# Optimization experiments

Hardware: AMD Instinct MI355X
Metric: run time of the kernel (lower is better)

## Reference

```python
import jax, jax.numpy as jnp
import numpy as np

N = 50000   # nodes
E = 400000  # edges (before self-loops)
F = 128     # num_features
H = 8       # heads (layer 1)
C = 64      # hidden_channels
B = 64      # graphs in batch
K = 10      # num_classes
NEG_SLOPE = 0.2


def setup_inputs() -> dict:
    key = jax.random.key(0)
    ks = jax.random.split(key, 12)
    g = lambda k, shape, fan: jax.random.normal(k, shape, jnp.float32) / np.sqrt(fan).astype(np.float32)
    return {
        "x": jax.random.normal(ks[0], (N, F), jnp.float32),
        "edge_index": jax.random.randint(ks[1], (2, E), 0, N, jnp.int32),
        "batch": jnp.sort(jax.random.randint(ks[2], (N,), 0, B, jnp.int32)),
        "W1": g(ks[3], (F, H * C), F),
        "att_src1": g(ks[4], (H, C), C),
        "att_dst1": g(ks[5], (H, C), C),
        "b1": jnp.zeros((H * C,), jnp.float32),
        "W2": g(ks[6], (H * C, C), H * C),
        "att_src2": g(ks[7], (1, C), C),
        "att_dst2": g(ks[8], (1, C), C),
        "b2": jnp.zeros((C,), jnp.float32),
        "lin1_w": g(ks[9], (C, C), C),
        "lin1_b": jnp.zeros((C,), jnp.float32),
        "lin2_w": g(ks[10], (C, K), C),
        "lin2_b": jnp.zeros((K,), jnp.float32),
    }


def gat_conv(x, src, dst, W, att_src, att_dst, bias):
    """PyG GATConv (self-loops already appended to src/dst). x:[N,Fin] -> [N,H*C]."""
    heads, out_c = att_src.shape
    h = (x @ W).reshape(N, heads, out_c)                      # [N,H,C]
    a_s = jnp.einsum('nhc,hc->nh', h, att_src)                # [N,H]
    a_d = jnp.einsum('nhc,hc->nh', h, att_dst)
    e = jax.nn.leaky_relu(a_s[src] + a_d[dst], NEG_SLOPE)     # [E',H]
    # segment softmax over incoming edges of each destination node
    m = jax.ops.segment_max(e, dst, num_segments=N)
    e = jnp.exp(e - m[dst])
    denom = jax.ops.segment_sum(e, dst, num_segments=N)
    alpha = e / (denom[dst] + 1e-16)                          # [E',H]
    out = jax.ops.segment_sum(h[src] * alpha[:, :, None], dst, num_segments=N)  # [N,H,C]
    return out.reshape(N, heads * out_c) + bias


def reference(x, edge_index, batch, W1, att_src1, att_dst1, b1,
              W2, att_src2, att_dst2, b2, lin1_w, lin1_b, lin2_w, lin2_b):
    loops = jnp.arange(N, dtype=edge_index.dtype)
    src = jnp.concatenate([edge_index[0], loops])
    dst = jnp.concatenate([edge_index[1], loops])

    h = gat_conv(x, src, dst, W1, att_src1, att_dst1, b1)     # [N, H*C]
    h = jax.nn.elu(h)                                         # dropout inactive (eval)
    h = gat_conv(h, src, dst, W2, att_src2, att_dst2, b2)     # [N, C]
    h = jax.nn.elu(h)

    pooled = jax.ops.segment_sum(h, batch, num_segments=B)    # global_add_pool -> [B, C]
    z = jax.nn.elu(pooled @ lin1_w + lin1_b)
    logits = z @ lin2_w + lin2_b
    return jax.nn.log_softmax(logits, axis=-1)
```

## Files before the change

### kernel.cpp

```cpp
#include <hip/hip_runtime.h>
#include <hip/hip_bf16.h>

#define DEV static __device__ __forceinline__

constexpr int F1 = 128;
constexpr int H1 = 8;
constexpr int C  = 64;
constexpr int B  = 64;
constexpr int K  = 10;
constexpr float NEG = 0.2f;
constexpr unsigned SMASK = 0x07FFFFFFu;

typedef __attribute__((ext_vector_type(8))) short short8;
typedef __attribute__((ext_vector_type(4))) float floatx4;

DEV float b2f(__hip_bfloat16 x) { return __bfloat162float(x); }
DEV float elu1(float v) { return v > 0.f ? v : (__expf(v) - 1.f); }
DEV unsigned short f2bbits(float f) {
  __hip_bfloat16 b = __float2bfloat16(f);
  return *(unsigned short*)&b;
}
DEV float blo(unsigned u) { return __uint_as_float(u << 16); }
DEV float bhi(unsigned u) { return __uint_as_float(u & 0xffff0000u); }
DEV float bu(unsigned short u) { return __uint_as_float(((unsigned)u) << 16); }
DEV unsigned pack2(float lo, float hi) {
  return (unsigned)f2bbits(lo) | ((unsigned)f2bbits(hi) << 16);
}
DEV float rcp_nr(float x) {
  float r = __builtin_amdgcn_rcpf(x);
  return r * (2.f - x * r);
}


DEV int detect_dev(const void* xraw, int* lds) {
  if (threadIdx.x == 0) {
    const __hip_bfloat16* xb = (const __hip_bfloat16*)xraw;
    int bad = 0;
    for (int i = 0; i < 128; ++i) {
      float v = b2f(xb[2 * i]);
      if (!(fabsf(v) < 1e4f)) bad++;
    }
    *lds = (bad < 13) ? 1 : 0;
  }
  __syncthreads();
  return *lds;
}

#define CVT(p, i) (isbf ? b2f(((const __hip_bfloat16*)(p))[i]) : ((const float*)(p))[i])

__global__ void fused_prep_kernel(const void* x_raw, const void* w1raw,
                                  const void* as1r, const void* ad1r, const void* b1r,
                                  const void* w2raw,
                                  const void* as2r, const void* ad2r, const void* b2r,
                                  const void* l1wr, const void* l1br,
                                  const void* l2wr, const void* l2br,
                                  unsigned short* __restrict__ xbf,
                                  unsigned short* __restrict__ w1frag,
                                  unsigned short* __restrict__ w2frag,
                                  unsigned short* __restrict__ vfrag,
                                  float* __restrict__ wts,
                                  int* __restrict__ deg,
                                  float* __restrict__ pooled,
                                  int nX, int N) {
  __shared__ int fl;
  int isbf = detect_dev(x_raw, &fl);
  int gid = blockIdx.x * 256 + threadIdx.x;
  int stride = gridDim.x * 256;

  int ng = nX >> 3;
  if (isbf) {
    const uint4* src = (const uint4*)x_raw;
    uint4* dst = (uint4*)xbf;
    for (int i = gid; i < ng; i += stride) dst[i] = src[i];
  } else {
    const float4* src = (const float4*)x_raw;
    uint4* dst = (uint4*)xbf;
    for (int i = gid; i < ng; i += stride) {
      float4 a = src[2 * i], b = src[2 * i + 1];
      uint4 o;
      o.x = pack2(a.x, a.y); o.y = pack2(a.z, a.w);
      o.z = pack2(b.x, b.y); o.w = pack2(b.z, b.w);
      dst[i] = o;
    }
  }
  for (int i = ng * 8 + gid; i < nX; i += stride)
    xbf[i] = isbf ? ((const unsigned short*)x_raw)[i]
                  : f2bbits(((const float*)x_raw)[i]);

  for (int i = gid; i < 512;  i += stride) {
    int hp = i >> 7, l16 = (i >> 3) & 15, nt = i & 7;
    int c = hp * 128 + nt * 16 + l16;
    wts[1024 + i] = CVT(b1r, c);
  }
  for (int i = gid; i < 64;   i += stride) wts[1536 + i] = CVT(as2r, i);
  for (int i = gid; i < 64;   i += stride) wts[1600 + i] = CVT(ad2r, i);
  for (int i = gid; i < 64;   i += stride) wts[1664 + i] = CVT(b2r, i);
  for (int i = gid; i < 4096; i += stride) wts[1728 + i] = CVT(l1wr, i);
  for (int i = gid; i < 64;   i += stride) wts[5824 + i] = CVT(l1br, i);
  for (int i = gid; i < 640;  i += stride) wts[5888 + i] = CVT(l2wr, i);
  for (int i = gid; i < 10;   i += stride) wts[6528 + i] = CVT(l2br, i);
  for (int t = gid; t < 8192; t += stride) {
    int lane = t & 63, ks = (t >> 6) & 3, nt = t >> 8;
    for (int j = 0; j < 8; ++j) {
      int k = ks * 32 + (lane >> 4) * 8 + j;
      int n = nt * 16 + (lane & 15);
      w1frag[t * 8 + j] = f2bbits(CVT(w1raw, k * 512 + n));
    }
  }
  for (int t = gid; t < 4096; t += stride) {
    int lane = t & 63, nt = (t >> 6) & 3, ks = t >> 8;
    for (int j = 0; j < 8; ++j) {
      int p = ks * 32 + (lane >> 4) * 8 + j;
      int hp = p >> 7, pl16 = (p >> 3) & 15, pnt = p & 7;
      int k = hp * 128 + pnt * 16 + pl16;
      int n = nt * 16 + (lane & 15);
      w2frag[t * 8 + j] = f2bbits(CVT(w2raw, k * 64 + n));
    }
  }
  for (int t = gid; t < 2048; t += stride) {
    int j = t & 7, lane = (t >> 3) & 63, ks = t >> 9;
    int k = ks * 32 + (lane >> 4) * 8 + j;
    int n = lane & 15;
    int hh = (n < 8) ? n : (n - 8);
    float s = 0.f;
    if (n < 8) {
      for (int c = 0; c < 64; ++c)
        s += CVT(w1raw, k * 512 + hh * 64 + c) * CVT(as1r, hh * 64 + c);
    } else {
      for (int c = 0; c < 64; ++c)
        s += CVT(w1raw, k * 512 + hh * 64 + c) * CVT(ad1r, hh * 64 + c);
    }
    vfrag[(ks * 64 + lane) * 8 + j] = f2bbits(s);
  }
  for (int i = gid; i < N; i += stride) deg[i] = 0;
  for (int i = gid; i < B * C; i += stride) pooled[i] = 0.f;
}

__global__ __launch_bounds__(256) void deg_att_kernel(
    const int* __restrict__ ei, int E, int Etot, int* __restrict__ deg,
    const unsigned short* __restrict__ xbf,
    const unsigned short* __restrict__ vfrag,
    float* __restrict__ a_s, float* __restrict__ a_d,
    int N, int attBlocks) {
  if ((int)blockIdx.x >= attBlocks) {
    int e = ((int)blockIdx.x - attBlocks) * 256 + threadIdx.x;
    if (e < Etot) {
      int d = (e < E) ? ei[E + e] : e - E;
      atomicAdd(&deg[d], 1);
    }
    return;
  }
  int t = threadIdx.x, w = t >> 6, lane = t & 63;
  int quad = lane >> 4, l16 = lane & 15;
  int row0 = blockIdx.x * 64 + w * 16;

  floatx4 acc = {};
  int rl = row0 + l16; if (rl >= N) rl = N - 1;
  const unsigned short* xp = xbf + (size_t)rl * 128 + quad * 8;
#pragma unroll
  for (int ks = 0; ks < 4; ++ks) {
    short8 a = *(const short8*)(xp + ks * 32);
    short8 b = *(const short8*)&vfrag[(ks * 64 + lane) * 8];
    acc = __builtin_amdgcn_mfma_f32_16x16x32_bf16(a, b, acc, 0, 0, 0);
  }
#pragma unroll
  for (int r = 0; r < 4; ++r) {
    int row = row0 + quad * 4 + r;
    if (row < N) {
      if (l16 < 8) a_s[(size_t)row * 8 + l16] = acc[r];
      else         a_d[(size_t)row * 8 + (l16 - 8)] = acc[r];
    }
  }
}

__global__ void scan_block_kernel(const int* __restrict__ deg,
                                  int* __restrict__ local,
                                  int* __restrict__ bsum, int N) {
  __shared__ int tmp[256];
  int t = threadIdx.x;
  int i = blockIdx.x * 256 + t;
  int v = (i < N) ? deg[i] : 0;
  tmp[t] = v;
  __syncthreads();
  for (int off = 1; off < 256; off <<= 1) {
    int u = (t >= off) ? tmp[t - off] : 0;
    __syncthreads();
    tmp[t] += u;
    __syncthreads();
  }
  if (i < N) local[i] = tmp[t] - v;
  if (t == 255) bsum[blockIdx.x] = tmp[255];
}

__global__ void scan_finish_kernel(const int* __restrict__ local,
                                   const int* __restrict__ bsum, int nb,
                                   int* __restrict__ rowptr,
                                   int* __restrict__ cursor, int N, int Etot) {
  __shared__ int tmp[256];
  __shared__ int offs;
  int t = threadIdx.x;
  int v0 = (t < nb) ? bsum[t] : 0;
  tmp[t] = v0;
  __syncthreads();
  for (int off = 1; off < 256; off <<= 1) {
    int u = (t >= off) ? tmp[t - off] : 0;
    __syncthreads();
    tmp[t] += u;
    __syncthreads();
  }
  if (t == (int)blockIdx.x) offs = tmp[t] - v0;
  __syncthreads();
  int i = blockIdx.x * 256 + t;
  if (i < N) {
    int r = local[i] + offs;
    rowptr[i] = r;
    cursor[i] = r;
  }
  if (i == 0) rowptr[N] = Etot;
}

__global__ void fill_weight_kernel(const int* __restrict__ ei, int E, int Etot,
                                   const float* __restrict__ a_s,
                                   const float* __restrict__ a_d,
                                   int* __restrict__ cursor,
                                   int* __restrict__ col,
                                   unsigned short* __restrict__ wedge) {
  int e = blockIdx.x * 256 + threadIdx.x;
  if (e >= Etot) return;
  int s, d;
  if (e < E) { s = ei[e]; d = ei[E + e]; } else { s = d = e - E; }
  int pos = atomicAdd(&cursor[d], 1);
  col[pos] = s | ((d & 15) << 27);
  float4 s0 = *(const float4*)(a_s + (size_t)s * 8);
  float4 s1 = *(const float4*)(a_s + (size_t)s * 8 + 4);
  float4 d0 = *(const float4*)(a_d + (size_t)d * 8);
  float4 d1 = *(const float4*)(a_d + (size_t)d * 8 + 4);
  float v, w0, w1, w2, w3, w4, w5, w6, w7;
  v = s0.x + d0.x; v = v > 0.f ? v : NEG * v; w0 = __expf(v);
  v = s0.y + d0.y; v = v > 0.f ? v : NEG * v; w1 = __expf(v);
  v = s0.z + d0.z; v = v > 0.f ? v : NEG * v; w2 = __expf(v);
  v = s0.w + d0.w; v = v > 0.f ? v : NEG * v; w3 = __expf(v);
  v = s1.x + d1.x; v = v > 0.f ? v : NEG * v; w4 = __expf(v);
  v = s1.y + d1.y; v = v > 0.f ? v : NEG * v; w5 = __expf(v);
  v = s1.z + d1.z; v = v > 0.f ? v : NEG * v; w6 = __expf(v);
  v = s1.w + d1.w; v = v > 0.f ? v : NEG * v; w7 = __expf(v);
  uint4 o;
  o.x = pack2(w0, w1); o.y = pack2(w2, w3);
  o.z = pack2(w4, w5); o.w = pack2(w6, w7);
  *(uint4*)(wedge + (size_t)pos * 8) = o;
}

__global__ __launch_bounds__(512, 6) void aggx_gemm12_kernel(
    const unsigned short* __restrict__ xbf,
    const unsigned short* __restrict__ W1frag,
    const int* __restrict__ rowptr,
    const int* __restrict__ col,
    const unsigned short* __restrict__ wedge,
    const float* __restrict__ bias_perm,
    const unsigned short* __restrict__ W2frag,
    const float* __restrict__ att_src2,
    const float* __restrict__ att_dst2,
    unsigned short* __restrict__ h2,
    float* __restrict__ a_s2, float* __restrict__ a_d2,
    int N) {
  __shared__ __align__(16) char LB[8 * 16 * 136 * 2];

  int t = threadIdx.x, w = t >> 6, lane = t & 63;
  int q = lane >> 4, n = lane & 15;
  int dbase = blockIdx.x * 16;

  int R0 = rowptr[dbase];
  int R1 = rowptr[min(dbase + 16, N)];
  int nch = (R1 - R0 + 31) >> 5;

  int kp = t >> 5, pp = t & 31;
  int skey = (pp & 7) << 4;
  int dw = t >> 5, kw = t & 31;

  short8 onesf = {};
  if (n == 0) {
#pragma unroll
    for (int j = 0; j < 8; ++j) onesf[j] = (short)0x3F80;
  }

  floatx4 accw[8] = {};
  floatx4 accdn = {};

  uint2 pxa, pxb;
  uint4 pwv;
  int pcv;
  {
    int e0 = R0 + 2 * kp;
    int ec0 = min(e0, R1 - 1), ec1 = min(e0 + 1, R1 - 1);
    int s0 = col[ec0] & SMASK;
    int s1 = col[ec1] & SMASK;
    pxa = *(const uint2*)(xbf + (size_t)s0 * 128 + pp * 4);
    pxb = *(const uint2*)(xbf + (size_t)s1 * 128 + pp * 4);
    int ew = min(R0 + kw, R1 - 1);
    pcv = col[ew];
    pwv = *(const uint4*)(wedge + (size_t)ew * 8);
  }

  for (int c = 0; c < nch; ++c) {
    char* Lb = LB + (c & 1) * 16384;
    unsigned short* XgTc = (unsigned short*)Lb;
    unsigned short* Wmc  = (unsigned short*)(Lb + 8192);

    {
      int base = 256 * pp + 4 * kp;
      unsigned w0 = (pxa.x & 0xffffu) | (pxb.x << 16);
      unsigned w1 = (pxa.x >> 16) | (pxb.x & 0xffff0000u);
      unsigned w2 = (pxa.y & 0xffffu) | (pxb.y << 16);
      unsigned w3 = (pxa.y >> 16) | (pxb.y & 0xffff0000u);
      *(unsigned*)(Lb + ((base)       ^ skey)) = w0;
      *(unsigned*)(Lb + ((base + 64)  ^ skey)) = w1;
      *(unsigned*)(Lb + ((base + 128) ^ skey)) = w2;
      *(unsigned*)(Lb + ((base + 192) ^ skey)) = w3;

      int ew = R0 + c * 32 + kw;
      int dl = (pcv >> 27) & 15;
      bool mine = (ew < R1) && (dl == dw);
      unsigned short* wmp = Wmc + dw * 32 + kw;
      wmp[0]    = mine ? (unsigned short)(pwv.x & 0xffff) : 0;
      wmp[512]  = mine ? (unsigned short)(pwv.x >> 16)    : 0;
      wmp[1024] = mine ? (unsigned short)(pwv.y & 0xffff) : 0;
      wmp[1536] = mine ? (unsigned short)(pwv.y >> 16)    : 0;
      wmp[2048] = mine ? (unsigned short)(pwv.z & 0xffff) : 0;
      wmp[2560] = mine ? (unsigned short)(pwv.z >> 16)    : 0;
      wmp[3072] = mine ? (unsigned short)(pwv.w & 0xffff) : 0;
      wmp[3584] = mine ? (unsigned short)(pwv.w >> 16)    : 0;
    }
    if (c + 1 < nch) {
      int ebase = R0 + (c + 1) * 32;
      int e0 = ebase + 2 * kp;
      int ec0 = min(e0, R1 - 1), ec1 = min(e0 + 1, R1 - 1);
      int s0 = col[ec0] & SMASK;
      int s1 = col[ec1] & SMASK;
      pxa = *(const uint2*)(xbf + (size_t)s0 * 128 + pp * 4);
      pxb = *(const uint2*)(xbf + (size_t)s1 * 128 + pp * 4);
      int ew = min(ebase + kw, R1 - 1);
      pcv = col[ew];
      pwv = *(const uint4*)(wedge + (size_t)ew * 8);
    }
    __syncthreads();

    short8 af = *(const short8*)(Wmc + w * 512 + n * 32 + 8 * q);
    accdn = __builtin_amdgcn_mfma_f32_16x16x32_bf16(af, onesf, accdn, 0, 0, 0);
#pragma unroll
    for (int ft = 0; ft < 8; ++ft) {
      int f = ft * 16 + n;
      int bb = f * 64 + 16 * q;
      bb ^= ((f >> 2) & 7) << 4;
      short8 bfr = *(const short8*)((const char*)XgTc + bb);
      accw[ft] = __builtin_amdgcn_mfma_f32_16x16x32_bf16(af, bfr, accw[ft], 0, 0, 0);
    }
  }

  __syncthreads();

  unsigned short* AggP = (unsigned short*)LB;
  {
    float dnv[4];
#pragma unroll
    for (int r = 0; r < 4; ++r) {
      float dr = __shfl(accdn[r], lane & 48);
      dnv[r] = rcp_nr(dr + 1e-16f);
    }
#pragma unroll
    for (int ft = 0; ft < 8; ++ft)
#pragma unroll
      for (int r = 0; r < 4; ++r)
        AggP[w * 2176 + (4 * q + r) * 136 + ft * 16 + n] =
            f2bbits(accw[ft][r] * dnv[r]);
  }
  __syncthreads();

  int hp = w >> 1, qq = w & 1;
  floatx4 acc2[4] = {};
  {
    const unsigned short* Bp = W1frag + (size_t)hp * 16384;
#pragma unroll
    for (int ks = 0; ks < 4; ++ks) {
      short8 a2 = *(const short8*)&AggP[w * 2176 + n * 136 + ks * 32 + q * 8];
#pragma unroll
      for (int j = 0; j < 4; ++j) {
        int nt = qq * 4 + j;
        short8 b2 = *(const short8*)&Bp[((nt * 4 + ks) * 64 + lane) * 8];
        acc2[j] = __builtin_amdgcn_mfma_f32_16x16x32_bf16(a2, b2, acc2[j], 0, 0, 0);
      }
    }
  }
  float4 bq = *(const float4*)&bias_perm[hp * 128 + n * 8 + qq * 4];
  __syncthreads();

  unsigned short* O1 = (unsigned short*)LB;
  float* RED = (float*)(LB + 16640);
  float* PSb = (float*)(LB + 20736);
  float* PDb = (float*)(LB + 20800);

  {
#pragma unroll
    for (int r = 0; r < 4; ++r) {
      int dl = 4 * q + r;
      uint2 ov;
      ov.x = pack2(elu1(acc2[0][r] + bq.x), elu1(acc2[1][r] + bq.y));
      ov.y = pack2(elu1(acc2[2][r] + bq.z), elu1(acc2[3][r] + bq.w));
      *(uint2*)(O1 + dl * 520 + hp * 128 + n * 8 + qq * 4) = ov;
    }
    if (t < 32) ((float*)(LB + 20736))[t] = 0.f;
  }
  __syncthreads();

  int nt2 = w & 3, kh = w >> 2;
  floatx4 acc3 = {};
#pragma unroll
  for (int ks8 = 0; ks8 < 8; ++ks8) {
    int ks = kh * 8 + ks8;
    short8 a3 = *(const short8*)&O1[n * 520 + ks * 32 + q * 8];
    short8 b3 = *(const short8*)&W2frag[((ks * 4 + nt2) * 64 + lane) * 8];
    acc3 = __builtin_amdgcn_mfma_f32_16x16x32_bf16(a3, b3, acc3, 0, 0, 0);
  }
  if (kh == 1) *(floatx4*)&RED[(nt2 * 64 + lane) * 4] = acc3;
  __syncthreads();

  if (kh == 0) {
    floatx4 other = *(const floatx4*)&RED[(nt2 * 64 + lane) * 4];
    float asw = att_src2[nt2 * 16 + n];
    float adw = att_dst2[nt2 * 16 + n];
    float ps[4], pd[4];
#pragma unroll
    for (int r = 0; r < 4; ++r) {
      float v = acc3[r] + other[r];
      int row = dbase + 4 * q + r;
      if (row < N) h2[(size_t)row * 64 + nt2 * 16 + n] = f2bbits(v);
      ps[r] = v * asw;
      pd[r] = v * adw;
    }
#pragma unroll
    for (int r = 0; r < 4; ++r) {
      float p = ps[r], qd = pd[r];
#pragma unroll
      for (int off2 = 1; off2 < 16; off2 <<= 1) {
        p += __shfl_xor(p, off2);
        qd += __shfl_xor(qd, off2);
      }
      if (n == 0) {
        int dl = 4 * q + r;
        atomicAdd(&PSb[dl], p);
        atomicAdd(&PDb[dl], qd);
      }
    }
  }
  __syncthreads();
  if (t < 16) {
    int row = dbase + t;
    if (row < N) {
      a_s2[row] = PSb[t];
      a_d2[row] = PDb[t];
    }
  }
}

__global__ __launch_bounds__(256) void gat_agg1_pool_kernel(
    const int* __restrict__ rowptr,
    const int* __restrict__ col,
    const float* __restrict__ a_s,
    const float* __restrict__ a_d,
    const unsigned short* __restrict__ hfeat,
    const float* __restrict__ bias,
    const int* __restrict__ batch,
    float* __restrict__ pooled, int N) {
  __shared__ float S[16][64];
  int wave = threadIdx.x >> 6, lane = threadIdx.x & 63;
  int qg = lane >> 4, l16 = lane & 15;
  int base = blockIdx.x * 16;
  const uint2* hfu = (const uint2*)hfeat;
  float4 bb = ((const float4*)bias)[l16];

  for (int j = 0; j < 4; ++j) {
    int d = base + wave * 4 + j;
    if (d < N) {
      int beg = rowptr[d], end = rowptr[d + 1];
      float adv = a_d[d];
      float acc0 = 0.f, acc1 = 0.f, acc2 = 0.f, acc3 = 0.f, wsum = 0.f;
#pragma unroll 2
      for (int i = beg + qg; i < end; i += 4) {
        int s = col[i] & SMASK;
        float v = a_s[s] + adv;
        v = v > 0.f ? v : NEG * v;
        float wv = __expf(v);
        wsum += wv;
        uint2 u = hfu[(size_t)s * 16 + l16];
        acc0 += wv * blo(u.x); acc1 += wv * bhi(u.x);
        acc2 += wv * blo(u.y); acc3 += wv * bhi(u.y);
      }
#pragma unroll
      for (int off = 16; off <= 32; off <<= 1) {
        acc0 += __shfl_xor(acc0, off); acc1 += __shfl_xor(acc1, off);
        acc2 += __shfl_xor(acc2, off); acc3 += __shfl_xor(acc3, off);
        wsum += __shfl_xor(wsum, off);
      }
      float winv = 1.f / (wsum + 1e-16f);
      if (qg == 0) {
        int dl = wave * 4 + j;
        S[dl][4 * l16 + 0] = bu(f2bbits(elu1(acc0 * winv + bb.x)));
        S[dl][4 * l16 + 1] = bu(f2bbits(elu1(acc1 * winv + bb.y)));
        S[dl][4 * l16 + 2] = bu(f2bbits(elu1(acc2 * winv + bb.z)));
        S[dl][4 * l16 + 3] = bu(f2bbits(elu1(acc3 * winv + bb.w)));
      }
    }
  }
  __syncthreads();

  if (threadIdx.x < 64) {
    int ch = threadIdx.x;
    int cnt = min(16, N - base);
    if (cnt > 0) {
      int cur = batch[base];
      float acc = 0.f;
      for (int nn = 0; nn < cnt; ++nn) {
        int bn = batch[base + nn];
        if (bn != cur) {
          unsafeAtomicAdd(&pooled[cur * 64 + ch], acc);
          acc = 0.f; cur = bn;
        }
        acc += S[nn][ch];
      }
      unsafeAtomicAdd(&pooled[cur * 64 + ch], acc);
    }
  }
}

__global__ void head_kernel(const float* __restrict__ pooled,
                            const float* __restrict__ lin1_w,
                            const float* __restrict__ lin1_b,
                            const float* __restrict__ lin2_w,
                            const float* __restrict__ lin2_b,
                            const void* __restrict__ x_raw,
                            void* __restrict__ outv) {
  __shared__ float P[C];
  __shared__ float Zs[C];
  __shared__ float Ls[K];
  __shared__ float lse_s;
  __shared__ int fl;
  int isbf = detect_dev(x_raw, &fl);
  int g = blockIdx.x, t = threadIdx.x;
  P[t] = pooled[g * C + t];
  __syncthreads();
  float acc = lin1_b[t];
  for (int k = 0; k < C; ++k) acc += P[k] * lin1_w[k * C + t];
  Zs[t] = elu1(acc);
  __syncthreads();
  if (t < K) {
    float a = lin2_b[t];
    for (int k = 0; k < C; ++k) a += Zs[k] * lin2_w[k * K + t];
    Ls[t] = a;
  }
  __syncthreads();
  if (t == 0) {
    float mx = -1e30f;
    for (int c = 0; c < K; ++c) mx = fmaxf(mx, Ls[c]);
    float s = 0.f;
    for (int c = 0; c < K; ++c) s += __expf(Ls[c] - mx);
    lse_s = mx + __logf(s);
  }
  __syncthreads();
  if (t < K) {
    float val = Ls[t] - lse_s;
    if (isbf) ((__hip_bfloat16*)outv)[g * K + t] = __float2bfloat16(val);
    else      ((float*)outv)[g * K + t] = val;
  }
}

extern "C" void kernel_launch(void* const* d_in, const int* in_sizes, int n_in,
                              void* d_out, int out_size, void* d_ws, size_t ws_size,
                              hipStream_t stream) {
  const void* x_raw = d_in[0];
  const int*  ei    = (const int*)d_in[1];
  const int*  batch = (const int*)d_in[2];

  const int N    = in_sizes[2];
  const int E    = in_sizes[1] / 2;
  const int Etot = E + N;
  const int nb   = (N + 255) / 256;

  float* ws   = (float*)d_ws;
  size_t off  = 0;

  float* wts = ws + off; off += 6544;
  float* b1w  = wts + 1024;
  float* as2w = wts + 1536;
  float* ad2w = wts + 1600;
  float* b2w  = wts + 1664;
  float* l1w  = wts + 1728;
  float* l1b  = wts + 5824;
  float* l2w  = wts + 5888;
  float* l2b  = wts + 6528;

  unsigned short* xbf    = (unsigned short*)(ws + off); off += (size_t)N * 64;
  unsigned short* w1frag = (unsigned short*)(ws + off); off += 32768;
  unsigned short* w2frag = (unsigned short*)(ws + off); off += 16384;
  unsigned short* vfrag  = (unsigned short*)(ws + off); off += 1024;
  unsigned short* wedge  = (unsigned short*)(ws + off); off += (size_t)Etot * 4;
  unsigned short* h2bf   = (unsigned short*)(ws + off); off += (size_t)N * 32;
  float* as1  = ws + off; off += (size_t)N * H1;
  float* ad1  = ws + off; off += (size_t)N * H1;
  float* as2  = ws + off; off += (size_t)N;
  float* ad2  = ws + off; off += (size_t)N;
  float* pooled = ws + off; off += (size_t)B * C;

  int* ibase  = (int*)(ws + off);
  int* deg    = ibase;                 ibase += N;
  int* cursor = ibase;                 ibase += N;
  int* rowptr = ibase;                 ibase += N + 1;
  int* locals = ibase;                 ibase += N;
  int* bsum   = ibase;                 ibase += 256;
  int* col    = ibase;                 ibase += Etot;

  fused_prep_kernel<<<1024, 256, 0, stream>>>(
      x_raw, d_in[3], d_in[4], d_in[5], d_in[6], d_in[7], d_in[8], d_in[9],
      d_in[10], d_in[11], d_in[12], d_in[13], d_in[14],
      xbf, w1frag, w2frag, vfrag, wts, deg, pooled, in_sizes[0], N);

  {
    int attBlocks = (N + 63) / 64;
    int degBlocks = (Etot + 255) / 256;
    deg_att_kernel<<<attBlocks + degBlocks, 256, 0, stream>>>(
        ei, E, Etot, deg, xbf, vfrag, as1, ad1, N, attBlocks);
  }

  scan_block_kernel<<<nb, 256, 0, stream>>>(deg, locals, bsum, N);
  scan_finish_kernel<<<nb, 256, 0, stream>>>(locals, bsum, nb, rowptr, cursor, N, Etot);

  fill_weight_kernel<<<(Etot + 255) / 256, 256, 0, stream>>>(
      ei, E, Etot, as1, ad1, cursor, col, wedge);

  aggx_gemm12_kernel<<<(N + 15) / 16, 512, 0, stream>>>(
      xbf, w1frag, rowptr, col, wedge, b1w,
      w2frag, as2w, ad2w, h2bf, as2, ad2, N);

  gat_agg1_pool_kernel<<<(N + 15) / 16, 256, 0, stream>>>(
      rowptr, col, as2, ad2, h2bf, b2w, batch, pooled, N);

  head_kernel<<<B, 64, 0, stream>>>(pooled, l1w, l1b, l2w, l2b, x_raw, (void*)d_out);
}
```

Before: 268.3 us.

## Fuse two-pass prefix scan into one kernel with grid-wide atomic sync

Merges the block-scan and scan-finish kernels into one launch. The last block to finish computes the block prefixes serially, and the other blocks spin-wait on a flag. It also vectorizes the LDS transpose stores in the aggregation kernel, using a cross-half-wave shuffle so each lane writes two 64-bit stores instead of four 32-bit ones. This removes one kernel launch and the locals round-trip, but relies on all 196 blocks being co-resident for the spin-wait.

```diff
diff --git a/kernel.cpp b/kernel.cpp
--- a/kernel.cpp
+++ b/kernel.cpp
@@ -61,6 +61,7 @@
                                   float* __restrict__ wts,
                                   int* __restrict__ deg,
                                   float* __restrict__ pooled,
+                                  int* __restrict__ scansync,
                                   int nX, int N) {
   __shared__ int fl;
   int isbf = detect_dev(x_raw, &fl);
@@ -134,6 +135,7 @@
   }
   for (int i = gid; i < N; i += stride) deg[i] = 0;
   for (int i = gid; i < B * C; i += stride) pooled[i] = 0.f;
+  for (int i = gid; i < 2; i += stride) scansync[i] = 0;
 }
 
 __global__ __launch_bounds__(256) void deg_att_kernel(
@@ -173,12 +175,16 @@
   }
 }
 
-__global__ void scan_block_kernel(const int* __restrict__ deg,
-                                  int* __restrict__ local,
-                                  int* __restrict__ bsum, int N) {
+__global__ __launch_bounds__(256) void scan_fused_kernel(
+    const int* __restrict__ deg,
+    int* __restrict__ bsum, int* __restrict__ prefixes,
+    int* __restrict__ sync,
+    int* __restrict__ rowptr, int* __restrict__ cursor,
+    int N, int Etot, int nb) {
   __shared__ int tmp[256];
-  int t = threadIdx.x;
-  int i = blockIdx.x * 256 + t;
+  __shared__ int sprev;
+  int t = threadIdx.x, bid = blockIdx.x;
+  int i = bid * 256 + t;
   int v = (i < N) ? deg[i] : 0;
   tmp[t] = v;
   __syncthreads();
@@ -188,31 +194,36 @@
     tmp[t] += u;
     __syncthreads();
   }
-  if (i < N) local[i] = tmp[t] - v;
-  if (t == 255) bsum[blockIdx.x] = tmp[255];
-}
-
-__global__ void scan_finish_kernel(const int* __restrict__ local,
-                                   const int* __restrict__ bsum, int nb,
-                                   int* __restrict__ rowptr,
-                                   int* __restrict__ cursor, int N, int Etot) {
-  __shared__ int tmp[256];
-  __shared__ int offs;
-  int t = threadIdx.x;
-  int v0 = (t < nb) ? bsum[t] : 0;
-  tmp[t] = v0;
-  __syncthreads();
-  for (int off = 1; off < 256; off <<= 1) {
-    int u = (t >= off) ? tmp[t - off] : 0;
-    __syncthreads();
-    tmp[t] += u;
-    __syncthreads();
-  }
-  if (t == (int)blockIdx.x) offs = tmp[t] - v0;
-  __syncthreads();
-  int i = blockIdx.x * 256 + t;
+  int local_excl = tmp[t] - v;
+  if (t == 255) {
+    bsum[bid] = tmp[255];
+    __threadfence();
+  }
+  __syncthreads();
+  if (t == 0) {
+    int done = __hip_atomic_fetch_add(&sync[0], 1, __ATOMIC_ACQ_REL,
+                                      __HIP_MEMORY_SCOPE_AGENT);
+    if (done == nb - 1) {
+      int run = 0;
+      for (int j = 0; j < nb; ++j) {
+        int bv = __hip_atomic_load(&bsum[j], __ATOMIC_RELAXED,
+                                   __HIP_MEMORY_SCOPE_AGENT);
+        prefixes[j] = run;
+        run += bv;
+      }
+      __threadfence();
+      __hip_atomic_store(&sync[1], 1, __ATOMIC_RELEASE,
+                         __HIP_MEMORY_SCOPE_AGENT);
+    }
+    while (__hip_atomic_load(&sync[1], __ATOMIC_ACQUIRE,
+                             __HIP_MEMORY_SCOPE_AGENT) == 0)
+      __builtin_amdgcn_s_sleep(8);
+    sprev = __hip_atomic_load(&prefixes[bid], __ATOMIC_RELAXED,
+                              __HIP_MEMORY_SCOPE_AGENT);
+  }
+  __syncthreads();
   if (i < N) {
-    int r = local[i] + offs;
+    int r = local_excl + sprev;
     rowptr[i] = r;
     cursor[i] = r;
   }
@@ -307,15 +318,21 @@
     unsigned short* Wmc  = (unsigned short*)(Lb + 8192);
 
     {
-      int base = 256 * pp + 4 * kp;
       unsigned w0 = (pxa.x & 0xffffu) | (pxb.x << 16);
       unsigned w1 = (pxa.x >> 16) | (pxb.x & 0xffff0000u);
       unsigned w2 = (pxa.y & 0xffffu) | (pxb.y << 16);
       unsigned w3 = (pxa.y >> 16) | (pxb.y & 0xffff0000u);
-      *(unsigned*)(Lb + ((base)       ^ skey)) = w0;
-      *(unsigned*)(Lb + ((base + 64)  ^ skey)) = w1;
-      *(unsigned*)(Lb + ((base + 128) ^ skey)) = w2;
-      *(unsigned*)(Lb + ((base + 192) ^ skey)) = w3;
+      unsigned o0 = __shfl_xor(w0, 32);
+      unsigned o1 = __shfl_xor(w1, 32);
+      unsigned o2 = __shfl_xor(w2, 32);
+      unsigned o3 = __shfl_xor(w3, 32);
+      bool hi = lane >= 32;
+      uint2 da, db;
+      da.x = hi ? o2 : w0;  da.y = hi ? w2 : o0;
+      db.x = hi ? o3 : w1;  db.y = hi ? w3 : o1;
+      int ba = 256 * pp + (hi ? 128 : 0) + 8 * w;
+      *(uint2*)(Lb + ((ba)      ^ skey)) = da;
+      *(uint2*)(Lb + ((ba + 64) ^ skey)) = db;
 
       int ew = R0 + c * 32 + kw;
       int dl = (pcv >> 27) & 15;
@@ -613,14 +630,15 @@
   int* deg    = ibase;                 ibase += N;
   int* cursor = ibase;                 ibase += N;
   int* rowptr = ibase;                 ibase += N + 1;
-  int* locals = ibase;                 ibase += N;
   int* bsum   = ibase;                 ibase += 256;
+  int* prefixes = ibase;               ibase += 256;
+  int* scansync = ibase;               ibase += 2;
   int* col    = ibase;                 ibase += Etot;
 
   fused_prep_kernel<<<1024, 256, 0, stream>>>(
       x_raw, d_in[3], d_in[4], d_in[5], d_in[6], d_in[7], d_in[8], d_in[9],
       d_in[10], d_in[11], d_in[12], d_in[13], d_in[14],
-      xbf, w1frag, w2frag, vfrag, wts, deg, pooled, in_sizes[0], N);
+      xbf, w1frag, w2frag, vfrag, wts, deg, pooled, scansync, in_sizes[0], N);
 
   {
     int attBlocks = (N + 63) / 64;
@@ -629,8 +647,8 @@
         ei, E, Etot, deg, xbf, vfrag, as1, ad1, N, attBlocks);
   }
 
-  scan_block_kernel<<<nb, 256, 0, stream>>>(deg, locals, bsum, N);
-  scan_finish_kernel<<<nb, 256, 0, stream>>>(locals, bsum, nb, rowptr, cursor, N, Etot);
+  scan_fused_kernel<<<nb, 256, 0, stream>>>(deg, bsum, prefixes, scansync,
+                                            rowptr, cursor, N, Etot, nb);
 
   fill_weight_kernel<<<(Etot + 255) / 256, 256, 0, stream>>>(
       ei, E, Etot, as1, ad1, cursor, col, wedge);
```

Result: slower. 459.0 us (+71.1%).
